# Kernel tuning notes

Hardware: AMD Instinct MI355X
Metric: run time of the kernel (lower is better)

## Reference

```python
import jax, jax.numpy as jnp
import numpy as np

NUM_HEADS = 12


def setup_inputs() -> dict:
    key = jax.random.key(0)
    ks = jax.random.split(key, 10)
    B, S, H = 4, 1024, 768
    hd = H // NUM_HEADS
    hk = hv = 64
    scale = 1.0 / np.sqrt(H)
    inp = {
        "hidden_states": jax.random.normal(ks[0], (B, S, H), dtype=jnp.float32),
        "attention_mask": jnp.ones((B, S), dtype=jnp.float32),
        "Wq": jax.random.normal(ks[1], (H, H), dtype=jnp.float32) * scale,
        "bq": jnp.zeros((H,), dtype=jnp.float32),
        "Wk": jax.random.normal(ks[2], (H, H), dtype=jnp.float32) * scale,
        "bk": jnp.zeros((H,), dtype=jnp.float32),
        "Wv": jax.random.normal(ks[3], (H, H), dtype=jnp.float32) * scale,
        "bv": jnp.zeros((H,), dtype=jnp.float32),
        "E_key": jax.random.normal(ks[4], (2 * hk + 1, hd), dtype=jnp.float32) * 0.02,
        "E_val": jax.random.normal(ks[5], (2 * hv + 1, hd), dtype=jnp.float32) * 0.02,
    }
    return inp


def reference(hidden_states, attention_mask, Wq, bq, Wk, bk, Wv, bv, E_key, E_val):
    B, S, H = hidden_states.shape
    hd = H // NUM_HEADS

    def split_heads(x):  # [B,S,H] -> [B,nh,S,hd]
        return x.reshape(B, S, NUM_HEADS, hd).transpose(0, 2, 1, 3)

    q = split_heads(hidden_states @ Wq + bq)
    k = split_heads(hidden_states @ Wk + bk)
    v = split_heads(hidden_states @ Wv + bv)

    # content scores (note: original code applies NO 1/sqrt(d) scaling)
    scores = jnp.einsum("bhid,bhjd->bhij", q, k)

    # relative key-position scores: scores_pos[i,j] = q_i . E_key[j-i+hk] (banded)
    Rk = E_key.shape[0]
    hk = (Rk - 1) // 2
    rel = jnp.arange(S)[None, :] - jnp.arange(S)[:, None] + hk  # [S,S]
    valid_k = (rel >= 0) & (rel < Rk)
    p = jnp.einsum("bhid,rd->bhir", q, E_key)  # [B,nh,S,Rk]
    rel_c = jnp.clip(rel, 0, Rk - 1)
    scores_pos = jnp.take_along_axis(p, rel_c[None, None, :, :], axis=-1)
    scores = scores + jnp.where(valid_k[None, None], scores_pos, 0.0)

    # attention mask: (1 - m) * finfo.min added to scores
    ext = (1.0 - attention_mask[:, None, None, :]) * jnp.finfo(scores.dtype).min
    probs = jax.nn.softmax(scores + ext, axis=-1)

    ctx = jnp.einsum("bhij,bhjd->bhid", probs, v)

    # relative value-position: ctx_pos[i] = sum_j probs[i,j] * E_val[j-i+hv]
    Rv = E_val.shape[0]
    hv = (Rv - 1) // 2
    j_idx = jnp.arange(S)[:, None] + jnp.arange(Rv)[None, :] - hv  # [S,Rv]
    valid_v = (j_idx >= 0) & (j_idx < S)
    j_c = jnp.clip(j_idx, 0, S - 1)
    probs_band = jnp.take_along_axis(probs, j_c[None, None, :, :], axis=-1)
    probs_band = probs_band * valid_v[None, None].astype(probs.dtype)
    ctx = ctx + jnp.einsum("bhir,rd->bhid", probs_band, E_val)

    return ctx.transpose(0, 2, 1, 3).reshape(B, S, H)
```

## Files before the change

### kernel.cpp

```cpp
#include <hip/hip_runtime.h>
#include <hip/hip_bf16.h>
#include <math.h>

#define NH 12
#define SEQ 1024
#define HD 64
#define HDIM 768
#define BSZ 4
#define RK 129
#define FMIN -3.4028234663852886e38f

typedef __attribute__((ext_vector_type(8))) short short8;
typedef __attribute__((ext_vector_type(4))) short short4v;
typedef __attribute__((ext_vector_type(2))) unsigned uint2v;
typedef __attribute__((ext_vector_type(8))) _Float16 f16x8;
typedef __attribute__((ext_vector_type(4))) float f32x4;

__device__ inline short f2bf(float x) {
    union { __hip_bfloat16 h; short s; } u;
    u.h = __float2bfloat16(x);
    return u.s;
}
__device__ inline float bf2f(short s) {
    union { __hip_bfloat16 h; short t; } u;
    u.t = s;
    return __bfloat162float(u.h);
}
__device__ inline unsigned pk2(float a, float b) {
    return (unsigned)(unsigned short)f2bf(a) |
           ((unsigned)(unsigned short)f2bf(b) << 16);
}

__device__ inline void async_load16(void* lds, const void* g) {
    __builtin_amdgcn_global_load_lds(
        (const __attribute__((address_space(1))) unsigned int*)g,
        (__attribute__((address_space(3))) unsigned int*)lds, 16, 0, 0);
}

#define BAR()    asm volatile("s_barrier" ::: "memory")
#define WAITV0() asm volatile("s_waitcnt vmcnt(0)" ::: "memory")

#define NXCHUNK 393216
#define NECHUNK 1032
#define NEVCHUNK 1280
#define NCONVB ((NXCHUNK + NECHUNK + NEVCHUNK + 255) / 256)
#define NTRB   (144 * 3)
__global__ __launch_bounds__(256) void prep_kernel(
    const float* __restrict__ X, const float* __restrict__ Ek,
    const float* __restrict__ Ev,
    const float* __restrict__ Wq, const float* __restrict__ Wk, const float* __restrict__ Wv,
    _Float16* __restrict__ Xh, _Float16* __restrict__ Ekh, short* __restrict__ Evt,
    _Float16* __restrict__ Wtq, _Float16* __restrict__ Wtk, _Float16* __restrict__ Wtv)
{
    const int bidg = blockIdx.x;
    if (bidg < NCONVB) {
        int idx = bidg * 256 + threadIdx.x;
        if (idx < NXCHUNK + NECHUNK) {
            const float* src;
            _Float16* dst;
            if (idx < NXCHUNK) { src = X; dst = Xh; }
            else { idx -= NXCHUNK; src = Ek; dst = Ekh; }
            float4 a = ((const float4*)src)[idx * 2];
            float4 b = ((const float4*)src)[idx * 2 + 1];
            f16x8 o;
            o[0] = (_Float16)a.x; o[1] = (_Float16)a.y; o[2] = (_Float16)a.z; o[3] = (_Float16)a.w;
            o[4] = (_Float16)b.x; o[5] = (_Float16)b.y; o[6] = (_Float16)b.z; o[7] = (_Float16)b.w;
            ((f16x8*)dst)[idx] = o;
        } else if (idx < NXCHUNK + NECHUNK + NEVCHUNK) {
            idx -= NXCHUNK + NECHUNK;
            const int dim = idx / 20;
            const int r0  = (idx % 20) * 8;
            short8 o;
#pragma unroll
            for (int e = 0; e < 8; ++e) {
                int rel = r0 + e;
                float v = (rel < RK) ? Ev[(size_t)rel * HD + dim] : 0.0f;
                o[e] = f2bf(v);
            }
            *(short8*)&Evt[(size_t)dim * 160 + r0] = o;
        }
        return;
    }
    const int bid2 = bidg - NCONVB;
    const int z = bid2 / 144;
    const int r = bid2 % 144;
    const float* __restrict__ W = (z == 0) ? Wq : (z == 1) ? Wk : Wv;
    _Float16* __restrict__ Wt   = (z == 0) ? Wtq : (z == 1) ? Wtk : Wtv;

    __shared__ float sT[64][65];
    const int t  = threadIdx.x;
    const int k0 = (r / 12) * 64;
    const int n0 = (r % 12) * 64;

    const int c  = (t & 15) * 4;
    const int kr = t >> 4;
#pragma unroll
    for (int rr = 0; rr < 4; ++rr) {
        float4 v = *(const float4*)&W[(size_t)(k0 + kr + rr * 16) * HDIM + n0 + c];
        sT[c + 0][kr + rr * 16] = v.x;
        sT[c + 1][kr + rr * 16] = v.y;
        sT[c + 2][kr + rr * 16] = v.z;
        sT[c + 3][kr + rr * 16] = v.w;
    }
    __syncthreads();
    const int rn = t >> 2;
    const int ck = (t & 3) * 16;
#pragma unroll
    for (int g = 0; g < 2; ++g) {
        f16x8 o;
#pragma unroll
        for (int e = 0; e < 8; ++e) o[e] = (_Float16)sT[rn][ck + g * 8 + e];
        *(f16x8*)&Wt[(size_t)(n0 + rn) * HDIM + k0 + ck + g * 8] = o;
    }
}

__global__ __launch_bounds__(256) void qkv_mfma_kernel(
    const _Float16* __restrict__ Xh,
    const _Float16* __restrict__ Wtq, const _Float16* __restrict__ Wtk, const _Float16* __restrict__ Wtv,
    const float* __restrict__ bq, const float* __restrict__ bk, const float* __restrict__ bv,
    const float* __restrict__ maskg,
    _Float16* __restrict__ Qo, _Float16* __restrict__ Ko, short* __restrict__ Vt)
{
    int bid = blockIdx.x;
    bid = (bid & 7) * 72 + (bid >> 3);
    const int which = bid / 192;
    const int rem   = bid % 192;
    const int n0    = (rem / 32) * 128;
    const int m0    = (rem % 32) * 128;
    const _Float16* __restrict__ Wt = (which == 0) ? Wtq : (which == 1) ? Wtk : Wtv;
    const float* __restrict__ bias  = (which == 0) ? bq : (which == 1) ? bk : bv;

    __shared__ __align__(16) _Float16 sA[128 * 64];
    __shared__ __align__(16) _Float16 sB[128 * 64];

    const int t  = threadIdx.x;
    const int w  = t >> 6, l = t & 63;
    const int lq = l & 15, lg = l >> 4;
    const int wr = w >> 1, wc = w & 1;

    f32x4 acc[4][4];
#pragma unroll
    for (int i = 0; i < 4; ++i)
#pragma unroll
        for (int j = 0; j < 4; ++j) acc[i][j] = (f32x4){0.f, 0.f, 0.f, 0.f};

    for (int k0 = 0; k0 < HDIM; k0 += 64) {
        __syncthreads();
#pragma unroll
        for (int r = 0; r < 4; ++r) {
            const int cib = r * 256 + w * 64;
            const int ci  = cib + l;
            const int row = ci >> 3, cr = ci & 7;
            const int lc  = cr ^ (row & 7);
            async_load16(&sA[(size_t)cib * 8],
                         &Xh[(size_t)(m0 + row) * HDIM + k0 + lc * 8]);
            async_load16(&sB[(size_t)cib * 8],
                         &Wt[(size_t)(n0 + row) * HDIM + k0 + lc * 8]);
        }
        __syncthreads();

        f16x8 af[4][2], bf[4][2];
#pragma unroll
        for (int i = 0; i < 4; ++i) {
#pragma unroll
            for (int ks = 0; ks < 2; ++ks) {
                int ra = wr * 64 + i * 16 + lq;
                af[i][ks] = *(const f16x8*)((const char*)sA +
                            ra * 128 + ((ks * 64 + lg * 16) ^ ((ra & 7) << 4)));
                int rb = wc * 64 + i * 16 + lq;
                bf[i][ks] = *(const f16x8*)((const char*)sB +
                            rb * 128 + ((ks * 64 + lg * 16) ^ ((rb & 7) << 4)));
            }
        }
#pragma unroll
        for (int i = 0; i < 4; ++i)
#pragma unroll
            for (int j = 0; j < 4; ++j) {
                acc[i][j] = __builtin_amdgcn_mfma_f32_16x16x32_f16(af[i][0], bf[j][0], acc[i][j], 0, 0, 0);
                acc[i][j] = __builtin_amdgcn_mfma_f32_16x16x32_f16(af[i][1], bf[j][1], acc[i][j], 0, 0, 0);
            }
    }

    _Float16* __restrict__ Yh = (which == 0) ? Qo : Ko;
#pragma unroll
    for (int i = 0; i < 4; ++i) {
        const int mb = m0 + wr * 64 + i * 16 + lg * 4;
        const int bb = mb >> 10, ss = mb & 1023;
        float zz[4] = {1.f, 1.f, 1.f, 1.f};
        if (which == 2) {
            float4 mv = *(const float4*)&maskg[(size_t)bb * SEQ + ss];
            zz[0] = __expf((1.0f - mv.x) * FMIN);
            zz[1] = __expf((1.0f - mv.y) * FMIN);
            zz[2] = __expf((1.0f - mv.z) * FMIN);
            zz[3] = __expf((1.0f - mv.w) * FMIN);
        }
#pragma unroll
        for (int j = 0; j < 4; ++j) {
            const int n  = n0 + wc * 64 + j * 16 + lq;
            const float bv4 = bias[n];
            const int hh = n >> 6, dd = n & 63;
            if (which == 2) {
                short4v pk;
#pragma unroll
                for (int reg = 0; reg < 4; ++reg)
                    pk[reg] = f2bf((acc[i][j][reg] + bv4) * zz[reg]);
                *(short4v*)&Vt[((size_t)(bb * NH + hh) * HD + dd) * SEQ + ss] = pk;
            } else {
#pragma unroll
                for (int reg = 0; reg < 4; ++reg) {
                    const size_t off = ((size_t)(bb * NH + hh) * SEQ + ss + reg) * HD + dd;
                    Yh[off] = (_Float16)(acc[i][j][reg] + bv4);
                }
            }
        }
    }
}

__global__ __launch_bounds__(256, 3) void attn_mfma_kernel(
    const _Float16* __restrict__ Q, const _Float16* __restrict__ K,
    const short* __restrict__ Vt, const float* __restrict__ mask,
    const _Float16* __restrict__ Ekh, const short* __restrict__ Evt,
    float* __restrict__ out)
{
    __shared__ __align__(16) char smem[39424];
    _Float16* sPpos = (_Float16*)(smem + 20480);
    short*    sZ    = (short*)(smem + 37376);

    int bid = blockIdx.x;
    bid = (bid & 7) * 96 + (bid >> 3);
    const int bh = bid >> 4;
    const int i0 = (bid & 15) * 64;
    const int b  = bh / NH;
    const int h  = bh - b * NH;

    const int t  = threadIdx.x;
    const int w  = t >> 6;
    const int l  = t & 63;
    const int lq = l & 15;
    const int lg = l >> 4;
    const int wrow0 = i0 + w * 16;
    const int bt0 = ((wrow0 - 64 + 1024) >> 5) - 32;

    {
        const int krow = t >> 3, klc = (t & 7) ^ (krow & 7);
        async_load16(smem + t * 16, K + ((size_t)bh * SEQ + krow) * HD + klc * 8);
        const int vrow = t >> 2, vlc = (t & 3) ^ (vrow & 3);
        async_load16(smem + 8192 + t * 16, Vt + ((size_t)bh * HD + vrow) * SEQ + vlc * 8);
    }

    const _Float16* qp = Q + ((size_t)bh * SEQ + wrow0 + lq) * HD;
    f16x8 qf0 = *(const f16x8*)&qp[lg * 8];
    f16x8 qf1 = *(const f16x8*)&qp[32 + lg * 8];

#pragma unroll
    for (int nt = 0; nt < 9; ++nt) {
        int cc = nt * 16 + lq;
        f16x8 eb0 = {0, 0, 0, 0, 0, 0, 0, 0};
        f16x8 eb1 = {0, 0, 0, 0, 0, 0, 0, 0};
        if (cc < RK) {
            eb0 = *(const f16x8*)&Ekh[(size_t)cc * HD + lg * 8];
            eb1 = *(const f16x8*)&Ekh[(size_t)cc * HD + 32 + lg * 8];
        }
        f32x4 pc = {0.f, 0.f, 0.f, 0.f};
        pc = __builtin_amdgcn_mfma_f32_16x16x32_f16(qf0, eb0, pc, 0, 0, 0);
        pc = __builtin_amdgcn_mfma_f32_16x16x32_f16(qf1, eb1, pc, 0, 0, 0);
        if (cc < RK) {
#pragma unroll
            for (int reg = 0; reg < 4; ++reg)
                sPpos[(w * 16 + lg * 4 + reg) * 132 + cc] = (_Float16)pc[reg];
        }
    }

    {
        float4 mv = *(const float4*)&mask[(size_t)b * SEQ + t * 4];
        short4v zo;
        zo[0] = f2bf(__expf((1.0f - mv.x) * FMIN));
        zo[1] = f2bf(__expf((1.0f - mv.y) * FMIN));
        zo[2] = f2bf(__expf((1.0f - mv.z) * FMIN));
        zo[3] = f2bf(__expf((1.0f - mv.w) * FMIN));
        *(short4v*)&sZ[t * 4] = zo;
    }

    asm volatile("s_waitcnt vmcnt(0) lgkmcnt(0)" ::: "memory");
    BAR();

    f32x4 acc[4];
#pragma unroll
    for (int nt = 0; nt < 4; ++nt) acc[nt] = (f32x4){0.f, 0.f, 0.f, 0.f};
    f32x4 zacc = {0.f, 0.f, 0.f, 0.f};

    unsigned band[5][2][2];
#pragma unroll
    for (int s = 0; s < 5; ++s)
#pragma unroll
        for (int ct = 0; ct < 2; ++ct) { band[s][ct][0] = 0u; band[s][ct][1] = 0u; }

    const int ck0 = ((lg ^ (lq & 7)) << 4);
    const int ck1 = (((4 + lg) ^ (lq & 7)) << 4);
    char* sPw = smem + 16384 + w * 1024;
    const int pswz = (lq & 3) << 4;

    for (int jt = 0; jt < 32; ++jt) {
        const int cur = jt & 1;
        const int j0  = jt * 32;

        if (jt < 31) {
            const int jn0 = j0 + 32;
            const int krow = t >> 3, klc = (t & 7) ^ (krow & 7);
            async_load16(smem + (cur ^ 1) * 4096 + t * 16,
                         K + ((size_t)bh * SEQ + jn0 + krow) * HD + klc * 8);
            const int vrow = t >> 2, vlc = (t & 3) ^ (vrow & 3);
            async_load16(smem + 8192 + (cur ^ 1) * 4096 + t * 16,
                         Vt + ((size_t)bh * HD + vrow) * SEQ + jn0 + vlc * 8);
        }

        const char* sKc = smem + cur * 4096;
        f32x4 sc[2];
#pragma unroll
        for (int ct = 0; ct < 2; ++ct) {
            const int rb = (ct * 16 + lq) * 128;
            f16x8 kb0 = *(const f16x8*)(sKc + rb + ck0);
            f16x8 kb1 = *(const f16x8*)(sKc + rb + ck1);
            f32x4 s = {0.f, 0.f, 0.f, 0.f};
            s = __builtin_amdgcn_mfma_f32_16x16x32_f16(kb0, qf0, s, 0, 0, 0);
            s = __builtin_amdgcn_mfma_f32_16x16x32_f16(kb1, qf1, s, 0, 0, 0);
            sc[ct] = s;
        }

        float p[2][4];
        bool plain = true;
#pragma unroll
        for (int s = 0; s < 5; ++s) {
            if (jt == bt0 + s) {
                plain = false;
#pragma unroll
                for (int ct = 0; ct < 2; ++ct) {
                    const int kbase = j0 + ct * 16 + lg * 4;
                    const int relb  = kbase - wrow0 - lq + 64;
                    short4v zv4 = *(const short4v*)&sZ[kbase];
                    float bz[4];
#pragma unroll
                    for (int reg = 0; reg < 4; ++reg) {
                        float sv = sc[ct][reg];
                        const int rel = relb + reg;
                        const bool inb = ((unsigned)rel < (unsigned)RK);
                        if (inb) sv += (float)sPpos[(w * 16 + lq) * 132 + rel];
                        const float pv = __expf(sv);
                        p[ct][reg] = pv;
                        bz[reg] = pv * bf2f(zv4[reg]);
                    }
                    band[s][ct][0] = pk2(bz[0], bz[1]);
                    band[s][ct][1] = pk2(bz[2], bz[3]);
                }
            }
        }
        if (plain) {
#pragma unroll
            for (int ct = 0; ct < 2; ++ct)
#pragma unroll
                for (int reg = 0; reg < 4; ++reg)
                    p[ct][reg] = __expf(sc[ct][reg]);
        }

#pragma unroll
        for (int ct = 0; ct < 2; ++ct) {
            uint2v pw;
            pw[0] = pk2(p[ct][0], p[ct][1]);
            pw[1] = pk2(p[ct][2], p[ct][3]);
            *(uint2v*)(sPw + lq * 64 + ((ct * 32 + lg * 8) ^ pswz)) = pw;
        }

        short8 pa = *(const short8*)(sPw + lq * 64 + ((lg << 4) ^ pswz));
        short8 zb = *(const short8*)&sZ[j0 + lg * 8];
        zacc = __builtin_amdgcn_mfma_f32_16x16x32_bf16(pa, zb, zacc, 0, 0, 0);

        const char* sVc = smem + 8192 + cur * 4096;
#pragma unroll
        for (int nt = 0; nt < 4; ++nt) {
            short8 vb = *(const short8*)(sVc + (nt * 16 + lq) * 64 + ((lg ^ (lq & 3)) << 4));
            acc[nt] = __builtin_amdgcn_mfma_f32_16x16x32_bf16(pa, vb, acc[nt], 0, 0, 0);
        }

        WAITV0();
        BAR();
    }

    char* bandLds = smem + w * 5120;
    {
        short8 z8 = {0, 0, 0, 0, 0, 0, 0, 0};
#pragma unroll
        for (int i = 0; i < 5; ++i)
            *(short8*)(bandLds + l * 16 + i * 1024) = z8;
    }
#pragma unroll
    for (int s = 0; s < 5; ++s) {
        const int jts = bt0 + s;
        if ((unsigned)jts < 32u) {
#pragma unroll
            for (int ct = 0; ct < 2; ++ct)
#pragma unroll
                for (int hh = 0; hh < 2; ++hh) {
                    const unsigned pw = band[s][ct][hh];
                    const int k0v  = jts * 32 + ct * 16 + lg * 4 + hh * 2;
                    const int rel0 = k0v - wrow0 - lq + 64;
                    if ((unsigned)rel0 < (unsigned)RK)
                        *(short*)(bandLds + lq * 320 + rel0 * 2) = (short)(pw & 0xffff);
                    if ((unsigned)(rel0 + 1) < (unsigned)RK)
                        *(short*)(bandLds + lq * 320 + rel0 * 2 + 2) = (short)(pw >> 16);
                }
        }
    }

    short8 bandA[5];
#pragma unroll
    for (int ks = 0; ks < 5; ++ks)
        bandA[ks] = *(const short8*)(bandLds + lq * 320 + ks * 64 + lg * 16);
#pragma unroll
    for (int nt = 0; nt < 4; ++nt) {
#pragma unroll
        for (int ks = 0; ks < 5; ++ks) {
            short8 eb = *(const short8*)&Evt[(size_t)(nt * 16 + lq) * 160 + ks * 32 + lg * 8];
            acc[nt] = __builtin_amdgcn_mfma_f32_16x16x32_bf16(bandA[ks], eb, acc[nt], 0, 0, 0);
        }
    }

#pragma unroll
    for (int nt = 0; nt < 4; ++nt) {
#pragma unroll
        for (int reg = 0; reg < 4; ++reg) {
            int qi = wrow0 + lg * 4 + reg;
            out[((size_t)b * SEQ + qi) * HDIM + h * HD + nt * 16 + lq] =
                acc[nt][reg] / zacc[reg];
        }
    }
}

extern "C" void kernel_launch(void* const* d_in, const int* in_sizes, int n_in,
                              void* d_out, int out_size, void* d_ws, size_t ws_size,
                              hipStream_t stream) {
    const float* X    = (const float*)d_in[0];
    const float* mask = (const float*)d_in[1];
    const float* Wq   = (const float*)d_in[2];
    const float* bq   = (const float*)d_in[3];
    const float* Wk   = (const float*)d_in[4];
    const float* bk   = (const float*)d_in[5];
    const float* Wv   = (const float*)d_in[6];
    const float* bv   = (const float*)d_in[7];
    const float* Ek   = (const float*)d_in[8];
    const float* Ev   = (const float*)d_in[9];
    float* out        = (float*)d_out;

    char* ws = (char*)d_ws;
    const size_t SZ_QKV = (size_t)BSZ * NH * SEQ * HD * 2;
    const size_t SZ_W   = (size_t)HDIM * HDIM * 2;
    _Float16* Qh  = (_Float16*)(ws);
    _Float16* Kh  = (_Float16*)(ws + SZ_QKV);
    short*    Vt  = (short*)   (ws + 2 * SZ_QKV);
    _Float16* Xh  = (_Float16*)(ws + 3 * SZ_QKV);
    _Float16* Wtq = (_Float16*)(ws + 4 * SZ_QKV);
    _Float16* Wtk = (_Float16*)(ws + 4 * SZ_QKV + SZ_W);
    _Float16* Wtv = (_Float16*)(ws + 4 * SZ_QKV + 2 * SZ_W);
    _Float16* Ekh = (_Float16*)(ws + 4 * SZ_QKV + 3 * SZ_W);
    short*    Evt = (short*)   (ws + 4 * SZ_QKV + 3 * SZ_W + 20480);

    prep_kernel<<<NCONVB + NTRB, 256, 0, stream>>>(
        X, Ek, Ev, Wq, Wk, Wv, Xh, Ekh, Evt, Wtq, Wtk, Wtv);
    qkv_mfma_kernel<<<576, 256, 0, stream>>>(Xh, Wtq, Wtk, Wtv, bq, bk, bv, mask, Qh, Kh, Vt);
    attn_mfma_kernel<<<768, 256, 0, stream>>>(Qh, Kh, Vt, mask, Ekh, Evt, out);
}
```

Baseline: 92.26 us.

## Triple-buffer K/V tiles in attention and transpose V-projection MFMA for coalesced stores

```diff
diff --git a/kernel.cpp b/kernel.cpp
--- a/kernel.cpp
+++ b/kernel.cpp
@@ -39,6 +39,7 @@
 
 #define BAR()    asm volatile("s_barrier" ::: "memory")
 #define WAITV0() asm volatile("s_waitcnt vmcnt(0)" ::: "memory")
+#define WAITV2() asm volatile("s_waitcnt vmcnt(2)" ::: "memory")
 
 #define NXCHUNK 393216
 #define NECHUNK 1032
@@ -172,40 +173,54 @@
                             rb * 128 + ((ks * 64 + lg * 16) ^ ((rb & 7) << 4)));
             }
         }
-#pragma unroll
-        for (int i = 0; i < 4; ++i)
+        if (which == 2) {
+#pragma unroll
+            for (int i = 0; i < 4; ++i)
+#pragma unroll
+                for (int j = 0; j < 4; ++j) {
+                    acc[i][j] = __builtin_amdgcn_mfma_f32_16x16x32_f16(bf[j][0], af[i][0], acc[i][j], 0, 0, 0);
+                    acc[i][j] = __builtin_amdgcn_mfma_f32_16x16x32_f16(bf[j][1], af[i][1], acc[i][j], 0, 0, 0);
+                }
+        } else {
+#pragma unroll
+            for (int i = 0; i < 4; ++i)
+#pragma unroll
+                for (int j = 0; j < 4; ++j) {
+                    acc[i][j] = __builtin_amdgcn_mfma_f32_16x16x32_f16(af[i][0], bf[j][0], acc[i][j], 0, 0, 0);
+                    acc[i][j] = __builtin_amdgcn_mfma_f32_16x16x32_f16(af[i][1], bf[j][1], acc[i][j], 0, 0, 0);
+                }
+        }
+    }
+
+    if (which == 2) {
+#pragma unroll
+        for (int i = 0; i < 4; ++i) {
+            const int mm = m0 + wr * 64 + i * 16 + lq;
+            const int bb = mm >> 10, ss = mm & 1023;
+            const float zl = __expf((1.0f - maskg[(size_t)bb * SEQ + ss]) * FMIN);
 #pragma unroll
             for (int j = 0; j < 4; ++j) {
-                acc[i][j] = __builtin_amdgcn_mfma_f32_16x16x32_f16(af[i][0], bf[j][0], acc[i][j], 0, 0, 0);
-                acc[i][j] = __builtin_amdgcn_mfma_f32_16x16x32_f16(af[i][1], bf[j][1], acc[i][j], 0, 0, 0);
+                const int nb = n0 + wc * 64 + j * 16 + lg * 4;
+#pragma unroll
+                for (int reg = 0; reg < 4; ++reg) {
+                    const int nn = nb + reg;
+                    const int hh = nn >> 6, dd = nn & 63;
+                    Vt[((size_t)(bb * NH + hh) * HD + dd) * SEQ + ss] =
+                        f2bf((acc[i][j][reg] + bias[nn]) * zl);
+                }
             }
-    }
-
-    _Float16* __restrict__ Yh = (which == 0) ? Qo : Ko;
-#pragma unroll
-    for (int i = 0; i < 4; ++i) {
-        const int mb = m0 + wr * 64 + i * 16 + lg * 4;
-        const int bb = mb >> 10, ss = mb & 1023;
-        float zz[4] = {1.f, 1.f, 1.f, 1.f};
-        if (which == 2) {
-            float4 mv = *(const float4*)&maskg[(size_t)bb * SEQ + ss];
-            zz[0] = __expf((1.0f - mv.x) * FMIN);
-            zz[1] = __expf((1.0f - mv.y) * FMIN);
-            zz[2] = __expf((1.0f - mv.z) * FMIN);
-            zz[3] = __expf((1.0f - mv.w) * FMIN);
-        }
-#pragma unroll
-        for (int j = 0; j < 4; ++j) {
-            const int n  = n0 + wc * 64 + j * 16 + lq;
-            const float bv4 = bias[n];
-            const int hh = n >> 6, dd = n & 63;
-            if (which == 2) {
-                short4v pk;
-#pragma unroll
-                for (int reg = 0; reg < 4; ++reg)
-                    pk[reg] = f2bf((acc[i][j][reg] + bv4) * zz[reg]);
-                *(short4v*)&Vt[((size_t)(bb * NH + hh) * HD + dd) * SEQ + ss] = pk;
-            } else {
+        }
+    } else {
+        _Float16* __restrict__ Yh = (which == 0) ? Qo : Ko;
+#pragma unroll
+        for (int i = 0; i < 4; ++i) {
+            const int mb = m0 + wr * 64 + i * 16 + lg * 4;
+            const int bb = mb >> 10, ss = mb & 1023;
+#pragma unroll
+            for (int j = 0; j < 4; ++j) {
+                const int n  = n0 + wc * 64 + j * 16 + lq;
+                const float bv4 = bias[n];
+                const int hh = n >> 6, dd = n & 63;
 #pragma unroll
                 for (int reg = 0; reg < 4; ++reg) {
                     const size_t off = ((size_t)(bb * NH + hh) * SEQ + ss + reg) * HD + dd;
@@ -222,9 +237,9 @@
     const _Float16* __restrict__ Ekh, const short* __restrict__ Evt,
     float* __restrict__ out)
 {
-    __shared__ __align__(16) char smem[39424];
-    _Float16* sPpos = (_Float16*)(smem + 20480);
-    short*    sZ    = (short*)(smem + 37376);
+    __shared__ __align__(16) char smem[47616];
+    _Float16* sPpos = (_Float16*)(smem + 28672);
+    short*    sZ    = (short*)(smem + 45568);
 
     int bid = blockIdx.x;
     bid = (bid & 7) * 96 + (bid >> 3);
@@ -241,12 +256,15 @@
     const int wrow0 = i0 + w * 16;
     const int bt0 = ((wrow0 - 64 + 1024) >> 5) - 32;
 
-    {
-        const int krow = t >> 3, klc = (t & 7) ^ (krow & 7);
-        async_load16(smem + t * 16, K + ((size_t)bh * SEQ + krow) * HD + klc * 8);
-        const int vrow = t >> 2, vlc = (t & 3) ^ (vrow & 3);
-        async_load16(smem + 8192 + t * 16, Vt + ((size_t)bh * HD + vrow) * SEQ + vlc * 8);
-    }
+    const int krow = t >> 3, klc = (t & 7) ^ (krow & 7);
+    const int vrow = t >> 2, vlc = (t & 3) ^ (vrow & 3);
+    const _Float16* Ksrc = K + ((size_t)bh * SEQ + krow) * HD + klc * 8;
+    const short*    Vsrc = Vt + ((size_t)bh * HD + vrow) * SEQ + vlc * 8;
+
+    async_load16(smem + t * 16,          Ksrc);
+    async_load16(smem + 12288 + t * 16,  Vsrc);
+    async_load16(smem + 4096 + t * 16,   Ksrc + 32 * HD);
+    async_load16(smem + 16384 + t * 16,  Vsrc + 32);
 
     const _Float16* qp = Q + ((size_t)bh * SEQ + wrow0 + lq) * HD;
     f16x8 qf0 = *(const f16x8*)&qp[lg * 8];
@@ -281,7 +299,7 @@
         *(short4v*)&sZ[t * 4] = zo;
     }
 
-    asm volatile("s_waitcnt vmcnt(0) lgkmcnt(0)" ::: "memory");
+    asm volatile("s_waitcnt vmcnt(2) lgkmcnt(0)" ::: "memory");
     BAR();
 
     f32x4 acc[4];
@@ -297,30 +315,27 @@
 
     const int ck0 = ((lg ^ (lq & 7)) << 4);
     const int ck1 = (((4 + lg) ^ (lq & 7)) << 4);
-    char* sPw = smem + 16384 + w * 1024;
+    char* sPw = smem + 24576 + w * 1024;
     const int pswz = (lq & 3) << 4;
 
+    char* bK0 = smem;          char* bK1 = smem + 4096;  char* bK2 = smem + 8192;
+    char* bV0 = smem + 12288;  char* bV1 = smem + 16384; char* bV2 = smem + 20480;
+
     for (int jt = 0; jt < 32; ++jt) {
-        const int cur = jt & 1;
-        const int j0  = jt * 32;
-
-        if (jt < 31) {
-            const int jn0 = j0 + 32;
-            const int krow = t >> 3, klc = (t & 7) ^ (krow & 7);
-            async_load16(smem + (cur ^ 1) * 4096 + t * 16,
-                         K + ((size_t)bh * SEQ + jn0 + krow) * HD + klc * 8);
-            const int vrow = t >> 2, vlc = (t & 3) ^ (vrow & 3);
-            async_load16(smem + 8192 + (cur ^ 1) * 4096 + t * 16,
-                         Vt + ((size_t)bh * HD + vrow) * SEQ + jn0 + vlc * 8);
-        }
-
-        const char* sKc = smem + cur * 4096;
+        const int j0 = jt * 32;
+
+        if (jt < 30) {
+            const int jn0 = j0 + 64;
+            async_load16(bK2 + t * 16, Ksrc + (size_t)jn0 * HD);
+            async_load16(bV2 + t * 16, Vsrc + jn0);
+        }
+
         f32x4 sc[2];
 #pragma unroll
         for (int ct = 0; ct < 2; ++ct) {
             const int rb = (ct * 16 + lq) * 128;
-            f16x8 kb0 = *(const f16x8*)(sKc + rb + ck0);
-            f16x8 kb1 = *(const f16x8*)(sKc + rb + ck1);
+            f16x8 kb0 = *(const f16x8*)(bK0 + rb + ck0);
+            f16x8 kb1 = *(const f16x8*)(bK0 + rb + ck1);
             f32x4 s = {0.f, 0.f, 0.f, 0.f};
             s = __builtin_amdgcn_mfma_f32_16x16x32_f16(kb0, qf0, s, 0, 0, 0);
             s = __builtin_amdgcn_mfma_f32_16x16x32_f16(kb1, qf1, s, 0, 0, 0);
@@ -374,15 +389,18 @@
         short8 zb = *(const short8*)&sZ[j0 + lg * 8];
         zacc = __builtin_amdgcn_mfma_f32_16x16x32_bf16(pa, zb, zacc, 0, 0, 0);
 
-        const char* sVc = smem + 8192 + cur * 4096;
 #pragma unroll
         for (int nt = 0; nt < 4; ++nt) {
-            short8 vb = *(const short8*)(sVc + (nt * 16 + lq) * 64 + ((lg ^ (lq & 3)) << 4));
+            short8 vb = *(const short8*)(bV0 + (nt * 16 + lq) * 64 + ((lg ^ (lq & 3)) << 4));
             acc[nt] = __builtin_amdgcn_mfma_f32_16x16x32_bf16(pa, vb, acc[nt], 0, 0, 0);
         }
 
-        WAITV0();
+        if (jt < 30)       WAITV2();
+        else if (jt == 30) WAITV0();
         BAR();
+
+        char* tk = bK0; bK0 = bK1; bK1 = bK2; bK2 = tk;
+        char* tv = bV0; bV0 = bV1; bV1 = bV2; bV2 = tv;
     }
 
     char* bandLds = smem + w * 5120;
```

Measured after the change: 105.2 us. 1.14x slower.
